# Kernel tuning notes

Measured on AMD Instinct MI355X. Metric: run time of the kernel, lower is better.

## Reference

```python
import jax, jax.numpy as jnp
import numpy as np

WIN = 3      # win_h = win_w = 3 (required for the reshape in the original code)
DIL = 1      # dilation; unfold padding == dilation in the original module
CUT = 0.0    # self.cut is hard-set to 0 in __init__


def _l2norm(x):
    # torch F.normalize(dim=1, p=2): x / max(||x||_2, eps)
    n = jnp.sqrt(jnp.sum(x * x, axis=1, keepdims=True))
    return x / jnp.maximum(n, 1e-12)


def setup_inputs() -> dict:
    key = jax.random.key(0)
    k1, k2 = jax.random.split(key)
    image = jax.random.normal(k1, (4, 64, 256, 256), dtype=jnp.float32)
    event = jax.random.normal(k2, (4, 64, 256, 256), dtype=jnp.float32)
    return {"image": image, "event": event}


def reference(image, event):
    B, C, H, W = image.shape
    img = _l2norm(image)
    ev = _l2norm(event)

    pad = DIL  # unfold padding == dilation
    imgp = jnp.pad(img, ((0, 0), (0, 0), (pad, pad), (pad, pad)))

    # NOTE: the original code unfolds `image` for BOTH branches (event_neighbor
    # is also built from image) -- we reproduce that faithfully.
    outs = []
    for i in range(WIN):
        for j in range(WIN):
            if i == WIN // 2 and j == WIN // 2:
                continue  # center element (index num = win_h*win_w//2) dropped
            nb = imgp[:, :, i * DIL:i * DIL + H, j * DIL:j * DIL + W]  # [B,C,H,W]
            # sum over channels of (nb * img) * (nb * ev)
            outs.append(jnp.sum((nb * img) * (nb * ev), axis=1))  # [B,H,W]
    aff = jnp.stack(outs, axis=1)  # [B, win_h*win_w - 1, H, W]
    # affinity[affinity < cut] = cut with cut == 0
    return jnp.maximum(aff, CUT)
```

## Files before the change

### kernel.cpp

```cpp
#include <hip/hip_runtime.h>

#define NB 4
#define NC 64
#define NH 256
#define NW 256
#define HW (NH * NW)
#define CPW 16

__device__ __forceinline__ float4 f4zero() { return make_float4(0.f, 0.f, 0.f, 0.f); }

__global__ __launch_bounds__(256) void k_fused(
    const float* __restrict__ img, const float* __restrict__ ev,
    float* __restrict__ out)
{
    __shared__ float red[2][48][64];

    const int lane = threadIdx.x & 63;
    const int wv   = threadIdx.x >> 6;

    const int bid = blockIdx.x;
    const int swz = (bid & 7) * 128 + (bid >> 3);
    const int b = swz >> 8;
    const int h = swz & 255;
    const int w = lane << 2;

    const bool hm = (h > 0);
    const bool hp = (h < NH - 1);

    const size_t base = (size_t)b * NC * HW + (size_t)(wv * CPW) * HW
                      + (size_t)h * NW + w;
    const float* ibase = img + base;
    const float* ebase = ev + base;

    float acc[8][4];
    float si[3][4];
    float se[4];
#pragma unroll
    for (int k = 0; k < 8; ++k)
#pragma unroll
        for (int x = 0; x < 4; ++x) acc[k][x] = 0.f;
#pragma unroll
    for (int r = 0; r < 3; ++r)
#pragma unroll
        for (int x = 0; x < 4; ++x) si[r][x] = 0.f;
#pragma unroll
    for (int x = 0; x < 4; ++x) se[x] = 0.f;

#pragma unroll 2
    for (int c = 0; c < CPW; ++c) {
        const float* p = ibase + (size_t)c * HW;
        float4 zm = hm ? *(const float4*)(p - NW) : f4zero();
        float4 zz = *(const float4*)(p);
        float4 zp = hp ? *(const float4*)(p + NW) : f4zero();
        float4 ee = *(const float4*)(ebase + (size_t)c * HW);

        float lm = __shfl_up(zm.w, 1);
        float lz = __shfl_up(zz.w, 1);
        float lp = __shfl_up(zp.w, 1);
        float rm = __shfl_down(zm.x, 1);
        float rz = __shfl_down(zz.x, 1);
        float rp = __shfl_down(zp.x, 1);
        if (lane == 0)  { lm = 0.f; lz = 0.f; lp = 0.f; }
        if (lane == 63) { rm = 0.f; rz = 0.f; rp = 0.f; }

        float m6[6] = { lm, zm.x, zm.y, zm.z, zm.w, rm };
        float z6[6] = { lz, zz.x, zz.y, zz.z, zz.w, rz };
        float p6[6] = { lp, zp.x, zp.y, zp.z, zp.w, rp };
        float sqm[6], sqz[6], sqp[6];
#pragma unroll
        for (int i = 0; i < 6; ++i) {
            sqm[i] = m6[i] * m6[i];
            sqz[i] = z6[i] * z6[i];
            sqp[i] = p6[i] * p6[i];
        }
#pragma unroll
        for (int x = 0; x < 4; ++x) {
            si[0][x] += sqm[x + 1];
            si[1][x] += sqz[x + 1];
            si[2][x] += sqp[x + 1];
        }
        se[0] = fmaf(ee.x, ee.x, se[0]);
        se[1] = fmaf(ee.y, ee.y, se[1]);
        se[2] = fmaf(ee.z, ee.z, se[2]);
        se[3] = fmaf(ee.w, ee.w, se[3]);

        float pe[4] = { z6[1] * ee.x, z6[2] * ee.y, z6[3] * ee.z, z6[4] * ee.w };
#pragma unroll
        for (int x = 0; x < 4; ++x) {
            acc[0][x] = fmaf(sqm[x],     pe[x], acc[0][x]);
            acc[1][x] = fmaf(sqm[x + 1], pe[x], acc[1][x]);
            acc[2][x] = fmaf(sqm[x + 2], pe[x], acc[2][x]);
            acc[3][x] = fmaf(sqz[x],     pe[x], acc[3][x]);
            acc[4][x] = fmaf(sqz[x + 2], pe[x], acc[4][x]);
            acc[5][x] = fmaf(sqp[x],     pe[x], acc[5][x]);
            acc[6][x] = fmaf(sqp[x + 1], pe[x], acc[6][x]);
            acc[7][x] = fmaf(sqp[x + 2], pe[x], acc[7][x]);
        }
    }

    if (wv >= 2) {
        const int s = wv - 2;
#pragma unroll
        for (int k = 0; k < 8; ++k)
#pragma unroll
            for (int x = 0; x < 4; ++x) red[s][k * 4 + x][lane] = acc[k][x];
#pragma unroll
        for (int r = 0; r < 3; ++r)
#pragma unroll
            for (int x = 0; x < 4; ++x) red[s][32 + r * 4 + x][lane] = si[r][x];
#pragma unroll
        for (int x = 0; x < 4; ++x) red[s][44 + x][lane] = se[x];
    }
    __syncthreads();
    if (wv < 2) {
        const int s = wv;
#pragma unroll
        for (int k = 0; k < 8; ++k)
#pragma unroll
            for (int x = 0; x < 4; ++x) acc[k][x] += red[s][k * 4 + x][lane];
#pragma unroll
        for (int r = 0; r < 3; ++r)
#pragma unroll
            for (int x = 0; x < 4; ++x) si[r][x] += red[s][32 + r * 4 + x][lane];
#pragma unroll
        for (int x = 0; x < 4; ++x) se[x] += red[s][44 + x][lane];
    }
    __syncthreads();
    if (wv == 1) {
#pragma unroll
        for (int k = 0; k < 8; ++k)
#pragma unroll
            for (int x = 0; x < 4; ++x) red[0][k * 4 + x][lane] = acc[k][x];
#pragma unroll
        for (int r = 0; r < 3; ++r)
#pragma unroll
            for (int x = 0; x < 4; ++x) red[0][32 + r * 4 + x][lane] = si[r][x];
#pragma unroll
        for (int x = 0; x < 4; ++x) red[0][44 + x][lane] = se[x];
    }
    __syncthreads();
    if (wv != 0) return;

#pragma unroll
    for (int k = 0; k < 8; ++k)
#pragma unroll
        for (int x = 0; x < 4; ++x) acc[k][x] += red[0][k * 4 + x][lane];
#pragma unroll
    for (int r = 0; r < 3; ++r)
#pragma unroll
        for (int x = 0; x < 4; ++x) si[r][x] += red[0][32 + r * 4 + x][lane];
#pragma unroll
    for (int x = 0; x < 4; ++x) se[x] += red[0][44 + x][lane];

    float rnm[4], rnz[4], rnp[4], rne[4];
#pragma unroll
    for (int x = 0; x < 4; ++x) {
        rnm[x] = 1.f / fmaxf(sqrtf(si[0][x]), 1e-12f);
        rnz[x] = 1.f / fmaxf(sqrtf(si[1][x]), 1e-12f);
        rnp[x] = 1.f / fmaxf(sqrtf(si[2][x]), 1e-12f);
        rne[x] = 1.f / fmaxf(sqrtf(se[x]), 1e-12f);
    }

    float lnm = __shfl_up(rnm[3], 1);
    float lnz = __shfl_up(rnz[3], 1);
    float lnp = __shfl_up(rnp[3], 1);
    float rnm_ = __shfl_down(rnm[0], 1);
    float rnz_ = __shfl_down(rnz[0], 1);
    float rnp_ = __shfl_down(rnp[0], 1);
    if (lane == 0)  { lnm = 0.f; lnz = 0.f; lnp = 0.f; }
    if (lane == 63) { rnm_ = 0.f; rnz_ = 0.f; rnp_ = 0.f; }

    float nm6[6] = { lnm, rnm[0], rnm[1], rnm[2], rnm[3], rnm_ };
    float nz6[6] = { lnz, rnz[0], rnz[1], rnz[2], rnz[3], rnz_ };
    float np6[6] = { lnp, rnp[0], rnp[1], rnp[2], rnp[3], rnp_ };

    float ctr[4];
#pragma unroll
    for (int x = 0; x < 4; ++x) ctr[x] = nz6[x + 1] * rne[x];

    float* outp = out + (((size_t)b * 8) * NH + h) * NW + w;
#pragma unroll
    for (int k = 0; k < 8; ++k) {
        float nbv[4];
#pragma unroll
        for (int x = 0; x < 4; ++x) {
            float v;
            switch (k) {
                case 0: v = nm6[x];     break;
                case 1: v = nm6[x + 1]; break;
                case 2: v = nm6[x + 2]; break;
                case 3: v = nz6[x];     break;
                case 4: v = nz6[x + 2]; break;
                case 5: v = np6[x];     break;
                case 6: v = np6[x + 1]; break;
                default: v = np6[x + 2]; break;
            }
            nbv[x] = v;
        }
        float4 o;
        o.x = fmaxf(acc[k][0] * (nbv[0] * nbv[0]) * ctr[0], 0.f);
        o.y = fmaxf(acc[k][1] * (nbv[1] * nbv[1]) * ctr[1], 0.f);
        o.z = fmaxf(acc[k][2] * (nbv[2] * nbv[2]) * ctr[2], 0.f);
        o.w = fmaxf(acc[k][3] * (nbv[3] * nbv[3]) * ctr[3], 0.f);
        *(float4*)(outp + (size_t)k * NH * NW) = o;
    }
}

extern "C" void kernel_launch(void* const* d_in, const int* in_sizes, int n_in,
                              void* d_out, int out_size, void* d_ws, size_t ws_size,
                              hipStream_t stream) {
    (void)in_sizes; (void)n_in; (void)out_size; (void)d_ws; (void)ws_size;
    const float* img = (const float*)d_in[0];
    const float* ev  = (const float*)d_in[1];
    float* out = (float*)d_out;

    k_fused<<<NB * NH, 256, 0, stream>>>(img, ev, out);
}
```

Measured before the change: 29.74 us.

## Split each row into two half-width tiles with halo handling to double block count

Each block now covers half a row (128 columns) and each lane handles 2 pixels instead of 4, so the grid doubles to 2048 blocks. Edge lanes load halo columns from the neighbouring tile and also accumulate their squared norms, so neighbour normalisation is correct across the tile boundary. This is meant to raise occupancy and parallelism and cut register pressure. The cost is narrower float2 loads, extra scalar halo loads, and recomputing about three rows' worth of halo per tile.

```diff
diff --git a/kernel.cpp b/kernel.cpp
--- a/kernel.cpp
+++ b/kernel.cpp
@@ -7,86 +7,97 @@
 #define HW (NH * NW)
 #define CPW 16
 
-__device__ __forceinline__ float4 f4zero() { return make_float4(0.f, 0.f, 0.f, 0.f); }
+__device__ __forceinline__ float2 f2zero() { return make_float2(0.f, 0.f); }
+
+#define NV 30
 
 __global__ __launch_bounds__(256) void k_fused(
     const float* __restrict__ img, const float* __restrict__ ev,
     float* __restrict__ out)
 {
-    __shared__ float red[2][48][64];
+    __shared__ float red[2][NV][64];
 
     const int lane = threadIdx.x & 63;
     const int wv   = threadIdx.x >> 6;
 
     const int bid = blockIdx.x;
-    const int swz = (bid & 7) * 128 + (bid >> 3);
-    const int b = swz >> 8;
-    const int h = swz & 255;
-    const int w = lane << 2;
+    const int swz = (bid & 7) * 256 + (bid >> 3);
+    const int tile = swz & 1;
+    const int h    = (swz >> 1) & 255;
+    const int b    = swz >> 9;
+    const int w0   = tile * 128 + lane * 2;
 
     const bool hm = (h > 0);
     const bool hp = (h < NH - 1);
 
     const size_t base = (size_t)b * NC * HW + (size_t)(wv * CPW) * HW
-                      + (size_t)h * NW + w;
+                      + (size_t)h * NW + w0;
     const float* ibase = img + base;
     const float* ebase = ev + base;
 
-    float acc[8][4];
-    float si[3][4];
-    float se[4];
-#pragma unroll
-    for (int k = 0; k < 8; ++k)
-#pragma unroll
-        for (int x = 0; x < 4; ++x) acc[k][x] = 0.f;
-#pragma unroll
-    for (int r = 0; r < 3; ++r)
-#pragma unroll
-        for (int x = 0; x < 4; ++x) si[r][x] = 0.f;
-#pragma unroll
-    for (int x = 0; x < 4; ++x) se[x] = 0.f;
+    float acc[8][2];
+    float si[3][2];
+    float se[2];
+    float shl[3], shr[3];
+#pragma unroll
+    for (int k = 0; k < 8; ++k) { acc[k][0] = 0.f; acc[k][1] = 0.f; }
+#pragma unroll
+    for (int r = 0; r < 3; ++r) { si[r][0] = 0.f; si[r][1] = 0.f; shl[r] = 0.f; shr[r] = 0.f; }
+    se[0] = 0.f; se[1] = 0.f;
 
 #pragma unroll 2
     for (int c = 0; c < CPW; ++c) {
         const float* p = ibase + (size_t)c * HW;
-        float4 zm = hm ? *(const float4*)(p - NW) : f4zero();
-        float4 zz = *(const float4*)(p);
-        float4 zp = hp ? *(const float4*)(p + NW) : f4zero();
-        float4 ee = *(const float4*)(ebase + (size_t)c * HW);
-
-        float lm = __shfl_up(zm.w, 1);
-        float lz = __shfl_up(zz.w, 1);
-        float lp = __shfl_up(zp.w, 1);
+        float2 zm = hm ? *(const float2*)(p - NW) : f2zero();
+        float2 zz = *(const float2*)(p);
+        float2 zp = hp ? *(const float2*)(p + NW) : f2zero();
+        float2 ee = *(const float2*)(ebase + (size_t)c * HW);
+
+        float hlm = 0.f, hlz = 0.f, hlp = 0.f, hrm = 0.f, hrz = 0.f, hrp = 0.f;
+        if (tile == 1 && lane == 0) {
+            hlz = p[-1];
+            if (hm) hlm = p[-NW - 1];
+            if (hp) hlp = p[NW - 1];
+        }
+        if (tile == 0 && lane == 63) {
+            hrz = p[2];
+            if (hm) hrm = p[-NW + 2];
+            if (hp) hrp = p[NW + 2];
+        }
+
+        float lm = __shfl_up(zm.y, 1);
+        float lz = __shfl_up(zz.y, 1);
+        float lp = __shfl_up(zp.y, 1);
         float rm = __shfl_down(zm.x, 1);
         float rz = __shfl_down(zz.x, 1);
         float rp = __shfl_down(zp.x, 1);
-        if (lane == 0)  { lm = 0.f; lz = 0.f; lp = 0.f; }
-        if (lane == 63) { rm = 0.f; rz = 0.f; rp = 0.f; }
-
-        float m6[6] = { lm, zm.x, zm.y, zm.z, zm.w, rm };
-        float z6[6] = { lz, zz.x, zz.y, zz.z, zz.w, rz };
-        float p6[6] = { lp, zp.x, zp.y, zp.z, zp.w, rp };
-        float sqm[6], sqz[6], sqp[6];
-#pragma unroll
-        for (int i = 0; i < 6; ++i) {
-            sqm[i] = m6[i] * m6[i];
-            sqz[i] = z6[i] * z6[i];
-            sqp[i] = p6[i] * p6[i];
-        }
-#pragma unroll
-        for (int x = 0; x < 4; ++x) {
+        if (lane == 0)  { lm = hlm; lz = hlz; lp = hlp; }
+        if (lane == 63) { rm = hrm; rz = hrz; rp = hrp; }
+
+        float m4[4] = { lm, zm.x, zm.y, rm };
+        float z4[4] = { lz, zz.x, zz.y, rz };
+        float p4[4] = { lp, zp.x, zp.y, rp };
+        float sqm[4], sqz[4], sqp[4];
+#pragma unroll
+        for (int i = 0; i < 4; ++i) {
+            sqm[i] = m4[i] * m4[i];
+            sqz[i] = z4[i] * z4[i];
+            sqp[i] = p4[i] * p4[i];
+        }
+#pragma unroll
+        for (int x = 0; x < 2; ++x) {
             si[0][x] += sqm[x + 1];
             si[1][x] += sqz[x + 1];
             si[2][x] += sqp[x + 1];
         }
         se[0] = fmaf(ee.x, ee.x, se[0]);
         se[1] = fmaf(ee.y, ee.y, se[1]);
-        se[2] = fmaf(ee.z, ee.z, se[2]);
-        se[3] = fmaf(ee.w, ee.w, se[3]);
-
-        float pe[4] = { z6[1] * ee.x, z6[2] * ee.y, z6[3] * ee.z, z6[4] * ee.w };
-#pragma unroll
-        for (int x = 0; x < 4; ++x) {
+        shl[0] += sqm[0]; shl[1] += sqz[0]; shl[2] += sqp[0];
+        shr[0] += sqm[3]; shr[1] += sqz[3]; shr[2] += sqp[3];
+
+        float pe[2] = { z4[1] * ee.x, z4[2] * ee.y };
+#pragma unroll
+        for (int x = 0; x < 2; ++x) {
             acc[0][x] = fmaf(sqm[x],     pe[x], acc[0][x]);
             acc[1][x] = fmaf(sqm[x + 1], pe[x], acc[1][x]);
             acc[2][x] = fmaf(sqm[x + 2], pe[x], acc[2][x]);
@@ -98,111 +109,103 @@
         }
     }
 
-    if (wv >= 2) {
-        const int s = wv - 2;
-#pragma unroll
-        for (int k = 0; k < 8; ++k)
-#pragma unroll
-            for (int x = 0; x < 4; ++x) red[s][k * 4 + x][lane] = acc[k][x];
-#pragma unroll
-        for (int r = 0; r < 3; ++r)
-#pragma unroll
-            for (int x = 0; x < 4; ++x) red[s][32 + r * 4 + x][lane] = si[r][x];
-#pragma unroll
-        for (int x = 0; x < 4; ++x) red[s][44 + x][lane] = se[x];
-    }
+#define STORE_VALS(slot)                                                     \
+    {                                                                        \
+        for (int k = 0; k < 8; ++k) {                                        \
+            red[slot][k * 2 + 0][lane] = acc[k][0];                          \
+            red[slot][k * 2 + 1][lane] = acc[k][1];                          \
+        }                                                                    \
+        for (int r = 0; r < 3; ++r) {                                        \
+            red[slot][16 + r * 2 + 0][lane] = si[r][0];                      \
+            red[slot][16 + r * 2 + 1][lane] = si[r][1];                      \
+            red[slot][24 + r][lane] = shl[r];                                \
+            red[slot][27 + r][lane] = shr[r];                                \
+        }                                                                    \
+        red[slot][22][lane] = se[0];                                         \
+        red[slot][23][lane] = se[1];                                         \
+    }
+#define ADD_VALS(slot)                                                       \
+    {                                                                        \
+        for (int k = 0; k < 8; ++k) {                                        \
+            acc[k][0] += red[slot][k * 2 + 0][lane];                         \
+            acc[k][1] += red[slot][k * 2 + 1][lane];                         \
+        }                                                                    \
+        for (int r = 0; r < 3; ++r) {                                        \
+            si[r][0] += red[slot][16 + r * 2 + 0][lane];                     \
+            si[r][1] += red[slot][16 + r * 2 + 1][lane];                     \
+            shl[r] += red[slot][24 + r][lane];                               \
+            shr[r] += red[slot][27 + r][lane];                               \
+        }                                                                    \
+        se[0] += red[slot][22][lane];                                        \
+        se[1] += red[slot][23][lane];                                        \
+    }
+
+    if (wv >= 2) STORE_VALS(wv - 2);
     __syncthreads();
-    if (wv < 2) {
-        const int s = wv;
-#pragma unroll
-        for (int k = 0; k < 8; ++k)
-#pragma unroll
-            for (int x = 0; x < 4; ++x) acc[k][x] += red[s][k * 4 + x][lane];
-#pragma unroll
-        for (int r = 0; r < 3; ++r)
-#pragma unroll
-            for (int x = 0; x < 4; ++x) si[r][x] += red[s][32 + r * 4 + x][lane];
-#pragma unroll
-        for (int x = 0; x < 4; ++x) se[x] += red[s][44 + x][lane];
-    }
+    if (wv < 2) ADD_VALS(wv);
     __syncthreads();
-    if (wv == 1) {
-#pragma unroll
-        for (int k = 0; k < 8; ++k)
-#pragma unroll
-            for (int x = 0; x < 4; ++x) red[0][k * 4 + x][lane] = acc[k][x];
-#pragma unroll
-        for (int r = 0; r < 3; ++r)
-#pragma unroll
-            for (int x = 0; x < 4; ++x) red[0][32 + r * 4 + x][lane] = si[r][x];
-#pragma unroll
-        for (int x = 0; x < 4; ++x) red[0][44 + x][lane] = se[x];
-    }
+    if (wv == 1) STORE_VALS(0);
     __syncthreads();
     if (wv != 0) return;
-
-#pragma unroll
-    for (int k = 0; k < 8; ++k)
-#pragma unroll
-        for (int x = 0; x < 4; ++x) acc[k][x] += red[0][k * 4 + x][lane];
-#pragma unroll
-    for (int r = 0; r < 3; ++r)
-#pragma unroll
-        for (int x = 0; x < 4; ++x) si[r][x] += red[0][32 + r * 4 + x][lane];
-#pragma unroll
-    for (int x = 0; x < 4; ++x) se[x] += red[0][44 + x][lane];
-
-    float rnm[4], rnz[4], rnp[4], rne[4];
-#pragma unroll
-    for (int x = 0; x < 4; ++x) {
+    ADD_VALS(0);
+#undef STORE_VALS
+#undef ADD_VALS
+
+    float rnm[2], rnz[2], rnp[2], rnev[2];
+#pragma unroll
+    for (int x = 0; x < 2; ++x) {
         rnm[x] = 1.f / fmaxf(sqrtf(si[0][x]), 1e-12f);
         rnz[x] = 1.f / fmaxf(sqrtf(si[1][x]), 1e-12f);
         rnp[x] = 1.f / fmaxf(sqrtf(si[2][x]), 1e-12f);
-        rne[x] = 1.f / fmaxf(sqrtf(se[x]), 1e-12f);
-    }
-
-    float lnm = __shfl_up(rnm[3], 1);
-    float lnz = __shfl_up(rnz[3], 1);
-    float lnp = __shfl_up(rnp[3], 1);
+        rnev[x] = 1.f / fmaxf(sqrtf(se[x]), 1e-12f);
+    }
+    float rhl[3], rhr[3];
+#pragma unroll
+    for (int r = 0; r < 3; ++r) {
+        rhl[r] = 1.f / fmaxf(sqrtf(shl[r]), 1e-12f);
+        rhr[r] = 1.f / fmaxf(sqrtf(shr[r]), 1e-12f);
+    }
+
+    float lnm = __shfl_up(rnm[1], 1);
+    float lnz = __shfl_up(rnz[1], 1);
+    float lnp = __shfl_up(rnp[1], 1);
     float rnm_ = __shfl_down(rnm[0], 1);
     float rnz_ = __shfl_down(rnz[0], 1);
     float rnp_ = __shfl_down(rnp[0], 1);
-    if (lane == 0)  { lnm = 0.f; lnz = 0.f; lnp = 0.f; }
-    if (lane == 63) { rnm_ = 0.f; rnz_ = 0.f; rnp_ = 0.f; }
-
-    float nm6[6] = { lnm, rnm[0], rnm[1], rnm[2], rnm[3], rnm_ };
-    float nz6[6] = { lnz, rnz[0], rnz[1], rnz[2], rnz[3], rnz_ };
-    float np6[6] = { lnp, rnp[0], rnp[1], rnp[2], rnp[3], rnp_ };
-
-    float ctr[4];
-#pragma unroll
-    for (int x = 0; x < 4; ++x) ctr[x] = nz6[x + 1] * rne[x];
-
-    float* outp = out + (((size_t)b * 8) * NH + h) * NW + w;
+    if (lane == 0)  { lnm = rhl[0]; lnz = rhl[1]; lnp = rhl[2]; }
+    if (lane == 63) { rnm_ = rhr[0]; rnz_ = rhr[1]; rnp_ = rhr[2]; }
+
+    float nm4[4] = { lnm, rnm[0], rnm[1], rnm_ };
+    float nz4[4] = { lnz, rnz[0], rnz[1], rnz_ };
+    float np4[4] = { lnp, rnp[0], rnp[1], rnp_ };
+
+    float ctr[2];
+#pragma unroll
+    for (int x = 0; x < 2; ++x) ctr[x] = nz4[x + 1] * rnev[x];
+
+    float* outp = out + (((size_t)b * 8) * NH + h) * NW + w0;
 #pragma unroll
     for (int k = 0; k < 8; ++k) {
-        float nbv[4];
-#pragma unroll
-        for (int x = 0; x < 4; ++x) {
+        float nbv[2];
+#pragma unroll
+        for (int x = 0; x < 2; ++x) {
             float v;
             switch (k) {
-                case 0: v = nm6[x];     break;
-                case 1: v = nm6[x + 1]; break;
-                case 2: v = nm6[x + 2]; break;
-                case 3: v = nz6[x];     break;
-                case 4: v = nz6[x + 2]; break;
-                case 5: v = np6[x];     break;
-                case 6: v = np6[x + 1]; break;
-                default: v = np6[x + 2]; break;
+                case 0: v = nm4[x];     break;
+                case 1: v = nm4[x + 1]; break;
+                case 2: v = nm4[x + 2]; break;
+                case 3: v = nz4[x];     break;
+                case 4: v = nz4[x + 2]; break;
+                case 5: v = np4[x];     break;
+                case 6: v = np4[x + 1]; break;
+                default: v = np4[x + 2]; break;
             }
             nbv[x] = v;
         }
-        float4 o;
+        float2 o;
         o.x = fmaxf(acc[k][0] * (nbv[0] * nbv[0]) * ctr[0], 0.f);
         o.y = fmaxf(acc[k][1] * (nbv[1] * nbv[1]) * ctr[1], 0.f);
-        o.z = fmaxf(acc[k][2] * (nbv[2] * nbv[2]) * ctr[2], 0.f);
-        o.w = fmaxf(acc[k][3] * (nbv[3] * nbv[3]) * ctr[3], 0.f);
-        *(float4*)(outp + (size_t)k * NH * NW) = o;
+        *(float2*)(outp + (size_t)k * NH * NW) = o;
     }
 }
 
@@ -214,5 +217,5 @@
     const float* ev  = (const float*)d_in[1];
     float* out = (float*)d_out;
 
-    k_fused<<<NB * NH, 256, 0, stream>>>(img, ev, out);
+    k_fused<<<NB * NH * 2, 256, 0, stream>>>(img, ev, out);
 }
```

Result: slower. 45.40 us (+52.7%).

## Stage 4-row image tiles in LDS via async global_load_lds with double buffering

Applied to the files above, without the earlier changes.

Each block now handles 4 output rows instead of 1. It stages a 6-row image halo plus 4 event rows per channel group into LDS using async global-to-LDS loads, double-buffered across 16 channel steps. This removes the roughly 3x redundant global reads of neighbour image rows and overlaps loading with compute. The cost is a barrier per channel step, a larger LDS footprint that may lower occupancy, and a shallower cross-wave reduction with two channel groups per row.

```diff
diff --git a/kernel.cpp b/kernel.cpp
--- a/kernel.cpp
+++ b/kernel.cpp
@@ -5,36 +5,43 @@
 #define NH 256
 #define NW 256
 #define HW (NH * NW)
-#define CPW 16
-
-__device__ __forceinline__ float4 f4zero() { return make_float4(0.f, 0.f, 0.f, 0.f); }
-
-__global__ __launch_bounds__(256) void k_fused(
+#define RPB 4
+#define CSTEP 4
+#define NSTEP (NC / CSTEP)
+
+__device__ __forceinline__ void gload_lds16(const float* g, float* l) {
+    __builtin_amdgcn_global_load_lds(
+        (const __attribute__((address_space(1))) void*)g,
+        (__attribute__((address_space(3))) void*)l, 16, 0, 0);
+}
+
+__global__ __launch_bounds__(512) void k_fused(
     const float* __restrict__ img, const float* __restrict__ ev,
     float* __restrict__ out)
 {
-    __shared__ float red[2][48][64];
+    __shared__ float lds[2][CSTEP][10][NW];
+    __shared__ float redbuf[RPB][48][64];
 
     const int lane = threadIdx.x & 63;
     const int wv   = threadIdx.x >> 6;
+    const int row  = wv >> 1;
+    const int g    = wv & 1;
 
     const int bid = blockIdx.x;
-    const int swz = (bid & 7) * 128 + (bid >> 3);
-    const int b = swz >> 8;
-    const int h = swz & 255;
-    const int w = lane << 2;
-
-    const bool hm = (h > 0);
-    const bool hp = (h < NH - 1);
-
-    const size_t base = (size_t)b * NC * HW + (size_t)(wv * CPW) * HW
-                      + (size_t)h * NW + w;
-    const float* ibase = img + base;
-    const float* ebase = ev + base;
-
-    float acc[8][4];
-    float si[3][4];
-    float se[4];
+    const int swz = (bid & 7) * 32 + (bid >> 3);
+    const int b   = swz >> 6;
+    const int h0  = (swz & 63) << 2;
+    const int h   = h0 + row;
+    const int w   = lane << 2;
+
+    const float hmf = (h > 0) ? 1.f : 0.f;
+    const float hpf = (h < NH - 1) ? 1.f : 0.f;
+
+    const size_t ibb = (size_t)b * NC * HW;
+    const float* gimg = img + ibb;
+    const float* gev  = ev + ibb;
+
+    float acc[8][4], si[3][4], se[4];
 #pragma unroll
     for (int k = 0; k < 8; ++k)
 #pragma unroll
@@ -46,111 +53,112 @@
 #pragma unroll
     for (int x = 0; x < 4; ++x) se[x] = 0.f;
 
-#pragma unroll 2
-    for (int c = 0; c < CPW; ++c) {
-        const float* p = ibase + (size_t)c * HW;
-        float4 zm = hm ? *(const float4*)(p - NW) : f4zero();
-        float4 zz = *(const float4*)(p);
-        float4 zp = hp ? *(const float4*)(p + NW) : f4zero();
-        float4 ee = *(const float4*)(ebase + (size_t)c * HW);
-
-        float lm = __shfl_up(zm.w, 1);
-        float lz = __shfl_up(zz.w, 1);
-        float lp = __shfl_up(zp.w, 1);
-        float rm = __shfl_down(zm.x, 1);
-        float rz = __shfl_down(zz.x, 1);
-        float rp = __shfl_down(zp.x, 1);
-        if (lane == 0)  { lm = 0.f; lz = 0.f; lp = 0.f; }
-        if (lane == 63) { rm = 0.f; rz = 0.f; rp = 0.f; }
-
-        float m6[6] = { lm, zm.x, zm.y, zm.z, zm.w, rm };
-        float z6[6] = { lz, zz.x, zz.y, zz.z, zz.w, rz };
-        float p6[6] = { lp, zp.x, zp.y, zp.z, zp.w, rp };
-        float sqm[6], sqz[6], sqp[6];
-#pragma unroll
-        for (int i = 0; i < 6; ++i) {
-            sqm[i] = m6[i] * m6[i];
-            sqz[i] = z6[i] * z6[i];
-            sqp[i] = p6[i] * p6[i];
-        }
-#pragma unroll
-        for (int x = 0; x < 4; ++x) {
-            si[0][x] += sqm[x + 1];
-            si[1][x] += sqz[x + 1];
-            si[2][x] += sqp[x + 1];
-        }
-        se[0] = fmaf(ee.x, ee.x, se[0]);
-        se[1] = fmaf(ee.y, ee.y, se[1]);
-        se[2] = fmaf(ee.z, ee.z, se[2]);
-        se[3] = fmaf(ee.w, ee.w, se[3]);
-
-        float pe[4] = { z6[1] * ee.x, z6[2] * ee.y, z6[3] * ee.z, z6[4] * ee.w };
-#pragma unroll
-        for (int x = 0; x < 4; ++x) {
-            acc[0][x] = fmaf(sqm[x],     pe[x], acc[0][x]);
-            acc[1][x] = fmaf(sqm[x + 1], pe[x], acc[1][x]);
-            acc[2][x] = fmaf(sqm[x + 2], pe[x], acc[2][x]);
-            acc[3][x] = fmaf(sqz[x],     pe[x], acc[3][x]);
-            acc[4][x] = fmaf(sqz[x + 2], pe[x], acc[4][x]);
-            acc[5][x] = fmaf(sqp[x],     pe[x], acc[5][x]);
-            acc[6][x] = fmaf(sqp[x + 1], pe[x], acc[6][x]);
-            acc[7][x] = fmaf(sqp[x + 2], pe[x], acc[7][x]);
-        }
-    }
-
-    if (wv >= 2) {
-        const int s = wv - 2;
+#define STAGE(snext)                                                         \
+    {                                                                        \
+        const int bufi_ = (snext) & 1;                                       \
+        _Pragma("unroll")                                                    \
+        for (int j = 0; j < 5; ++j) {                                        \
+            const int t  = wv * 5 + j;                                       \
+            const int cc = t / 10;                                           \
+            const int r  = t - cc * 10;                                      \
+            const int c  = (snext) * CSTEP + cc;                             \
+            const float* src;                                                \
+            if (r < 6) {                                                     \
+                int sr = h0 - 1 + r;                                         \
+                sr = sr < 0 ? 0 : (sr > NH - 1 ? NH - 1 : sr);               \
+                src = gimg + (size_t)c * HW + (size_t)sr * NW;               \
+            } else {                                                         \
+                src = gev + (size_t)c * HW + (size_t)(h0 + r - 6) * NW;      \
+            }                                                                \
+            gload_lds16(src + lane * 4, &lds[bufi_][cc][r][0]);              \
+        }                                                                    \
+    }
+
+#define COMPUTECH(bufi, cc)                                                  \
+    {                                                                        \
+        const float4* Mp = (const float4*)&lds[bufi][cc][row + 0][0];        \
+        const float4* Zp = (const float4*)&lds[bufi][cc][row + 1][0];        \
+        const float4* Pp = (const float4*)&lds[bufi][cc][row + 2][0];        \
+        const float4* Ep = (const float4*)&lds[bufi][cc][6 + row][0];        \
+        float4 M = Mp[lane], Z = Zp[lane], P = Pp[lane], E = Ep[lane];       \
+        M.x *= hmf; M.y *= hmf; M.z *= hmf; M.w *= hmf;                      \
+        P.x *= hpf; P.y *= hpf; P.z *= hpf; P.w *= hpf;                      \
+        float lm = __shfl_up(M.w, 1);                                        \
+        float lz = __shfl_up(Z.w, 1);                                        \
+        float lp = __shfl_up(P.w, 1);                                        \
+        float rm = __shfl_down(M.x, 1);                                      \
+        float rz = __shfl_down(Z.x, 1);                                      \
+        float rp = __shfl_down(P.x, 1);                                      \
+        if (lane == 0)  { lm = 0.f; lz = 0.f; lp = 0.f; }                    \
+        if (lane == 63) { rm = 0.f; rz = 0.f; rp = 0.f; }                    \
+        float m6[6] = { lm, M.x, M.y, M.z, M.w, rm };                        \
+        float z6[6] = { lz, Z.x, Z.y, Z.z, Z.w, rz };                        \
+        float p6[6] = { lp, P.x, P.y, P.z, P.w, rp };                        \
+        float sqm[6], sqz[6], sqp[6];                                        \
+        for (int i = 0; i < 6; ++i) {                                        \
+            sqm[i] = m6[i] * m6[i];                                          \
+            sqz[i] = z6[i] * z6[i];                                          \
+            sqp[i] = p6[i] * p6[i];                                          \
+        }                                                                    \
+        for (int x = 0; x < 4; ++x) {                                        \
+            si[0][x] += sqm[x + 1];                                          \
+            si[1][x] += sqz[x + 1];                                          \
+            si[2][x] += sqp[x + 1];                                          \
+        }                                                                    \
+        se[0] = fmaf(E.x, E.x, se[0]);                                       \
+        se[1] = fmaf(E.y, E.y, se[1]);                                       \
+        se[2] = fmaf(E.z, E.z, se[2]);                                       \
+        se[3] = fmaf(E.w, E.w, se[3]);                                       \
+        float pe[4] = { z6[1] * E.x, z6[2] * E.y, z6[3] * E.z, z6[4] * E.w };\
+        for (int x = 0; x < 4; ++x) {                                        \
+            acc[0][x] = fmaf(sqm[x],     pe[x], acc[0][x]);                  \
+            acc[1][x] = fmaf(sqm[x + 1], pe[x], acc[1][x]);                  \
+            acc[2][x] = fmaf(sqm[x + 2], pe[x], acc[2][x]);                  \
+            acc[3][x] = fmaf(sqz[x],     pe[x], acc[3][x]);                  \
+            acc[4][x] = fmaf(sqz[x + 2], pe[x], acc[4][x]);                  \
+            acc[5][x] = fmaf(sqp[x],     pe[x], acc[5][x]);                  \
+            acc[6][x] = fmaf(sqp[x + 1], pe[x], acc[6][x]);                  \
+            acc[7][x] = fmaf(sqp[x + 2], pe[x], acc[7][x]);                  \
+        }                                                                    \
+    }
+
+    STAGE(0);
+    __syncthreads();
+    for (int s = 0; s < NSTEP; ++s) {
+        if (s + 1 < NSTEP) STAGE(s + 1);
+        const int bufi = s & 1;
+        const int c0 = g * 2;
+        COMPUTECH(bufi, c0);
+        COMPUTECH(bufi, c0 + 1);
+        __syncthreads();
+    }
+#undef STAGE
+#undef COMPUTECH
+
+    if (g == 1) {
 #pragma unroll
         for (int k = 0; k < 8; ++k)
 #pragma unroll
-            for (int x = 0; x < 4; ++x) red[s][k * 4 + x][lane] = acc[k][x];
+            for (int x = 0; x < 4; ++x) redbuf[row][k * 4 + x][lane] = acc[k][x];
 #pragma unroll
         for (int r = 0; r < 3; ++r)
 #pragma unroll
-            for (int x = 0; x < 4; ++x) red[s][32 + r * 4 + x][lane] = si[r][x];
-#pragma unroll
-        for (int x = 0; x < 4; ++x) red[s][44 + x][lane] = se[x];
+            for (int x = 0; x < 4; ++x) redbuf[row][32 + r * 4 + x][lane] = si[r][x];
+#pragma unroll
+        for (int x = 0; x < 4; ++x) redbuf[row][44 + x][lane] = se[x];
     }
     __syncthreads();
-    if (wv < 2) {
-        const int s = wv;
-#pragma unroll
-        for (int k = 0; k < 8; ++k)
-#pragma unroll
-            for (int x = 0; x < 4; ++x) acc[k][x] += red[s][k * 4 + x][lane];
-#pragma unroll
-        for (int r = 0; r < 3; ++r)
-#pragma unroll
-            for (int x = 0; x < 4; ++x) si[r][x] += red[s][32 + r * 4 + x][lane];
-#pragma unroll
-        for (int x = 0; x < 4; ++x) se[x] += red[s][44 + x][lane];
-    }
-    __syncthreads();
-    if (wv == 1) {
-#pragma unroll
-        for (int k = 0; k < 8; ++k)
-#pragma unroll
-            for (int x = 0; x < 4; ++x) red[0][k * 4 + x][lane] = acc[k][x];
-#pragma unroll
-        for (int r = 0; r < 3; ++r)
-#pragma unroll
-            for (int x = 0; x < 4; ++x) red[0][32 + r * 4 + x][lane] = si[r][x];
-#pragma unroll
-        for (int x = 0; x < 4; ++x) red[0][44 + x][lane] = se[x];
-    }
-    __syncthreads();
-    if (wv != 0) return;
-
+    if (g == 1) return;
 #pragma unroll
     for (int k = 0; k < 8; ++k)
 #pragma unroll
-        for (int x = 0; x < 4; ++x) acc[k][x] += red[0][k * 4 + x][lane];
+        for (int x = 0; x < 4; ++x) acc[k][x] += redbuf[row][k * 4 + x][lane];
 #pragma unroll
     for (int r = 0; r < 3; ++r)
 #pragma unroll
-        for (int x = 0; x < 4; ++x) si[r][x] += red[0][32 + r * 4 + x][lane];
-#pragma unroll
-    for (int x = 0; x < 4; ++x) se[x] += red[0][44 + x][lane];
+        for (int x = 0; x < 4; ++x) si[r][x] += redbuf[row][32 + r * 4 + x][lane];
+#pragma unroll
+    for (int x = 0; x < 4; ++x) se[x] += redbuf[row][44 + x][lane];
 
     float rnm[4], rnz[4], rnp[4], rne[4];
 #pragma unroll
@@ -214,5 +222,5 @@
     const float* ev  = (const float*)d_in[1];
     float* out = (float*)d_out;
 
-    k_fused<<<NB * NH, 256, 0, stream>>>(img, ev, out);
+    k_fused<<<NB * (NH / RPB), 512, 0, stream>>>(img, ev, out);
 }
```

Result: slower. 32.38 us (+8.9%).
